# Performance work log

Measured on AMD Instinct MI355X. Metric: run time of the kernel, lower is better.

The kernel has to match this reference:

```python
import jax, jax.numpy as jnp
import numpy as np


def _relative_position_index(w):
    # Deterministic Swin relative-position index, shape [w*w, w*w], values in [0, (2w-1)^2)
    coords_h = np.arange(w)
    coords_w = np.arange(w)
    coords = np.stack(np.meshgrid(coords_h, coords_w, indexing="ij"))  # [2, w, w]
    coords = coords.reshape(2, -1)                                      # [2, w*w]
    rel = coords[:, :, None] - coords[:, None, :]                       # [2, N, N]
    rel = rel.transpose(1, 2, 0).copy()                                 # [N, N, 2]
    rel[:, :, 0] += w - 1
    rel[:, :, 1] += w - 1
    rel[:, :, 0] *= 2 * w - 1
    return jnp.asarray(rel.sum(-1), dtype=jnp.int32)


def setup_inputs() -> dict:
    key = jax.random.key(0)
    ks = jax.random.split(key, 7)
    BS, N, C, H, W = 4096, 49, 384, 12, 7
    NW = 64  # number of windows per image
    x = jax.random.normal(ks[0], (BS, N, C), dtype=jnp.float32)
    # Swin shift mask: 0 where attention allowed, -100 where blocked
    u = jax.random.uniform(ks[1], (NW, N, N))
    mask = jnp.where(u < 0.5, 0.0, -100.0).astype(jnp.float32)
    qkv_w = jax.random.normal(ks[2], (C, 3 * C), dtype=jnp.float32) * (C ** -0.5)
    qkv_b = jax.random.normal(ks[3], (3 * C,), dtype=jnp.float32) * 0.02
    proj_w = jax.random.normal(ks[4], (C, C), dtype=jnp.float32) * (C ** -0.5)
    proj_b = jax.random.normal(ks[5], (C,), dtype=jnp.float32) * 0.02
    bias_table = jax.random.normal(ks[6], ((2 * W - 1) ** 2, H), dtype=jnp.float32) * 0.02
    return {"x": x, "mask": mask, "qkv_w": qkv_w, "qkv_b": qkv_b,
            "proj_w": proj_w, "proj_b": proj_b, "bias_table": bias_table,
            "n_heads": 12, "window_size": 7}


def reference(x, mask, qkv_w, qkv_b, proj_w, proj_b, bias_table, n_heads, window_size):
    BS, N, C = x.shape
    Hh = n_heads
    hd = C // Hh
    scale = hd ** -0.5
    rpi = _relative_position_index(window_size)  # [N, N] int

    qkv = x @ qkv_w + qkv_b                       # [BS, N, 3C]
    qkv = qkv.reshape(BS, N, 3, Hh, hd).transpose(2, 0, 3, 1, 4)  # [3, BS, H, N, hd]
    q, k, v = qkv[0], qkv[1], qkv[2]

    attn = jnp.einsum("bhnd,bhmd->bhnm", q, k) * scale   # [BS, H, N, N]
    # relative position bias gather: [N*N, H] -> [H, N, N]
    rpb = bias_table[rpi.reshape(-1)].reshape(N, N, Hh).transpose(2, 0, 1)
    attn = attn + rpb[None]

    nw = mask.shape[0]
    attn = attn.reshape(BS // nw, nw, Hh, N, N) + mask[None, :, None]
    attn = attn.reshape(BS, Hh, N, N)

    attn = jax.nn.softmax(attn, axis=-1)
    out = jnp.einsum("bhnm,bhmd->bhnd", attn, v)          # [BS, H, N, hd]
    out = out.transpose(0, 2, 1, 3).reshape(BS, N, C)
    return out @ proj_w + proj_b
```

## Files before the change

### kernel.cpp

```cpp
#include <hip/hip_runtime.h>
#include <hip/hip_bf16.h>


typedef __attribute__((ext_vector_type(8))) short bf16x8;
typedef __attribute__((ext_vector_type(4))) float f32x4;

#define SEQ_N  49
#define CH     384
#define QKV_N  1152
#define HDIM   32
#define UNIT_ROWS 3136

__device__ __forceinline__ unsigned short f2b(float f) {
    union { float f; unsigned int u; } v; v.f = f;
    return (unsigned short)((v.u + 0x7FFFu + ((v.u >> 16) & 1u)) >> 16);
}

__device__ __forceinline__ bf16x8 ld8(const unsigned short* p) {
    return *(const bf16x8*)p;
}

__device__ __forceinline__ void gload16(const unsigned short* g, unsigned short* l) {
    __builtin_amdgcn_global_load_lds(
        (const __attribute__((address_space(1))) unsigned int*)g,
        (__attribute__((address_space(3))) unsigned int*)l, 16, 0, 0);
}

__device__ __forceinline__ int xcd_swizzle(int orig, int T) {
    int q = T >> 3, r = T & 7;
    int xcd = orig & 7, idx = orig >> 3;
    return (xcd < r ? xcd * (q + 1) : r * (q + 1) + (xcd - r) * q) + idx;
}

__global__ __launch_bounds__(256) void k_cvt_w(const float* __restrict__ wq,
        const float* __restrict__ wp, unsigned short* __restrict__ oq,
        unsigned short* __restrict__ op)
{
    int t = blockIdx.x * 256 + threadIdx.x;
    if (t < QKV_N * CH) {
        int n = t / CH, k = t - n * CH;
        oq[t] = f2b(wq[(size_t)k * QKV_N + n]);
    }
    if (t < CH * CH) {
        int n = t / CH, k = t - n * CH;
        op[t] = f2b(wp[(size_t)k * CH + n]);
    }
}

__global__ __launch_bounds__(256) void k_cvt(const float* __restrict__ in,
        unsigned short* __restrict__ outp, int n8)
{
    int stride = gridDim.x * 256;
    for (int i = blockIdx.x * 256 + threadIdx.x; i < n8; i += stride) {
        const float4* p = (const float4*)(in + (size_t)i * 8);
        float4 a = p[0], b = p[1];
        uint4 v;
        v.x = (unsigned)f2b(a.x) | ((unsigned)f2b(a.y) << 16);
        v.y = (unsigned)f2b(a.z) | ((unsigned)f2b(a.w) << 16);
        v.z = (unsigned)f2b(b.x) | ((unsigned)f2b(b.y) << 16);
        v.w = (unsigned)f2b(b.z) | ((unsigned)f2b(b.w) << 16);
        *(uint4*)(outp + (size_t)i * 8) = v;
    }
}

template<int OUTF32>
__global__ __launch_bounds__(256) void k_gemm(
        const unsigned short* __restrict__ A, int lda,
        const unsigned short* __restrict__ Bt, int K,
        const float* __restrict__ bias,
        unsigned short* __restrict__ Cb, float* __restrict__ Cf, int ldc,
        int M, int ntiles, int mtiles)
{
    __shared__ unsigned short As[128 * 32];
    __shared__ unsigned short Bs[128 * 32];
    const int wg = xcd_swizzle(blockIdx.x, mtiles * ntiles);
    const int m0 = (wg / ntiles) * 128;
    const int n0 = (wg % ntiles) * 128;
    const int tid = threadIdx.x;
    const int lane = tid & 63, wid = tid >> 6;
    const int wm = (wid >> 1) * 64, wn = (wid & 1) * 64;
    const int l15 = lane & 15, g = lane >> 4;

    f32x4 acc[4][4];
#pragma unroll
    for (int a = 0; a < 4; ++a)
#pragma unroll
        for (int b = 0; b < 4; ++b) acc[a][b] = (f32x4){0.f, 0.f, 0.f, 0.f};

    const int r0 = wid * 16 + (lane >> 2);
    const int kofs = (lane & 3) * 8;
    int ra0 = m0 + r0;       if (ra0 > M - 1) ra0 = M - 1;
    int ra1 = m0 + 64 + r0;  if (ra1 > M - 1) ra1 = M - 1;
    const unsigned short* a0p = A + (size_t)ra0 * lda + kofs;
    const unsigned short* a1p = A + (size_t)ra1 * lda + kofs;
    const unsigned short* b0p = Bt + (size_t)(n0 + r0) * K + kofs;
    const unsigned short* b1p = Bt + (size_t)(n0 + 64 + r0) * K + kofs;
    unsigned short* la0 = As + wid * 512;
    unsigned short* la1 = As + 2048 + wid * 512;
    unsigned short* lb0 = Bs + wid * 512;
    unsigned short* lb1 = Bs + 2048 + wid * 512;

    for (int kt = 0; kt < K; kt += 32) {
        gload16(a0p, la0);
        gload16(a1p, la1);
        gload16(b0p, lb0);
        gload16(b1p, lb1);
        a0p += 32; a1p += 32; b0p += 32; b1p += 32;
        __syncthreads();
        bf16x8 af[4], bfr[4];
#pragma unroll
        for (int mt = 0; mt < 4; ++mt)
            af[mt] = ld8(&As[(wm + mt * 16 + l15) * 32 + g * 8]);
#pragma unroll
        for (int nt = 0; nt < 4; ++nt)
            bfr[nt] = ld8(&Bs[(wn + nt * 16 + l15) * 32 + g * 8]);
#pragma unroll
        for (int mt = 0; mt < 4; ++mt)
#pragma unroll
            for (int nt = 0; nt < 4; ++nt)
                acc[mt][nt] = __builtin_amdgcn_mfma_f32_16x16x32_bf16(
                        af[mt], bfr[nt], acc[mt][nt], 0, 0, 0);
        __syncthreads();
    }

#pragma unroll
    for (int mt = 0; mt < 4; ++mt)
#pragma unroll
        for (int nt = 0; nt < 4; ++nt) {
            int col = n0 + wn + nt * 16 + l15;
            float bb = bias[col];
#pragma unroll
            for (int r = 0; r < 4; ++r) {
                int row = m0 + wm + mt * 16 + g * 4 + r;
                if (row < M) {
                    if (OUTF32)
                        Cf[(size_t)row * ldc + col] = acc[mt][nt][r] + bb;
                    else
                        Cb[(size_t)row * ldc + col] = f2b(acc[mt][nt][r] + bb);
                }
            }
        }
}

__global__ __launch_bounds__(256) void k_attn(unsigned short* __restrict__ qkv,
        const float* __restrict__ mask, const float* __restrict__ btab, int win_base)
{
    extern __shared__ unsigned short sm[];
    const int tid = threadIdx.x;
    const int lane = tid & 63, wv = tid >> 6;
    const int l15 = lane & 15, g = lane >> 4;
    const int pair = blockIdx.x * 4 + wv;
    const int winloc = pair / 12;
    const int h = pair - winloc * 12;
    const int wimg = (win_base + winloc) & 63;
    const int co = h * HDIM;
    unsigned short* Vt = sm + wv * 6912;
    unsigned short* Pw = Vt + 32 * 72;
    unsigned short* src = qkv + (size_t)winloc * SEQ_N * QKV_N;

    for (int t = lane; t < 32 * 16; t += 64) {
        int c = t >> 4, kk = 48 + (t & 15);
        Vt[c * 72 + kk] = 0;
    }
    for (int t = lane; t < 49 * 4; t += 64) {
        int row = t >> 2, cb = (t & 3) * 8;
        const unsigned short* vp = src + (size_t)row * QKV_N + 768 + co + cb;
        ushort4 a = ((const ushort4*)vp)[0];
        ushort4 b = ((const ushort4*)vp)[1];
        Vt[(cb + 0) * 72 + row] = a.x; Vt[(cb + 1) * 72 + row] = a.y;
        Vt[(cb + 2) * 72 + row] = a.z; Vt[(cb + 3) * 72 + row] = a.w;
        Vt[(cb + 4) * 72 + row] = b.x; Vt[(cb + 5) * 72 + row] = b.y;
        Vt[(cb + 6) * 72 + row] = b.z; Vt[(cb + 7) * 72 + row] = b.w;
    }

    bf16x8 qf[4], kf[4];
#pragma unroll
    for (int mt = 0; mt < 4; ++mt) {
        int r = mt * 16 + l15; if (r > 48) r = 48;
        qf[mt] = ld8(src + (size_t)r * QKV_N + co + g * 8);
    }
#pragma unroll
    for (int nt = 0; nt < 4; ++nt) {
        int r = nt * 16 + l15; if (r > 48) r = 48;
        kf[nt] = ld8(src + (size_t)r * QKV_N + CH + co + g * 8);
    }

    f32x4 sa[4][4];
#pragma unroll
    for (int mt = 0; mt < 4; ++mt)
#pragma unroll
        for (int nt = 0; nt < 4; ++nt) sa[mt][nt] = (f32x4){0.f, 0.f, 0.f, 0.f};
#pragma unroll
    for (int mt = 0; mt < 4; ++mt)
#pragma unroll
        for (int nt = 0; nt < 4; ++nt)
            sa[mt][nt] = __builtin_amdgcn_mfma_f32_16x16x32_bf16(
                    qf[mt], kf[nt], sa[mt][nt], 0, 0, 0);

    int jj[4], jh[4], jw4[4];
#pragma unroll
    for (int nt = 0; nt < 4; ++nt) {
        int j = nt * 16 + l15;
        jj[nt] = j; jh[nt] = j / 7; jw4[nt] = j - (j / 7) * 7;
    }
    const float scale = 0.17677669529663687f;
#pragma unroll
    for (int mt = 0; mt < 4; ++mt) {
#pragma unroll
        for (int r = 0; r < 4; ++r) {
            int i = mt * 16 + g * 4 + r;
            int ic = i < 49 ? i : 48;
            int ih = ic / 7, iw = ic - (ic / 7) * 7;
            const float* mrow = mask + (size_t)wimg * 2401 + ic * 49;
            float sv[4];
#pragma unroll
            for (int nt = 0; nt < 4; ++nt) {
                float s = sa[mt][nt][r];
                if (jj[nt] < 49) {
                    int idx = (ih - jh[nt] + 6) * 13 + (iw - jw4[nt] + 6);
                    s = s * scale + btab[idx * 12 + h] + mrow[jj[nt]];
                } else s = -1e30f;
                sv[nt] = s;
            }
            float mx = fmaxf(fmaxf(sv[0], sv[1]), fmaxf(sv[2], sv[3]));
#pragma unroll
            for (int d = 1; d < 16; d <<= 1) mx = fmaxf(mx, __shfl_xor(mx, d));
            float sum = 0.f;
#pragma unroll
            for (int nt = 0; nt < 4; ++nt) { sv[nt] = __expf(sv[nt] - mx); sum += sv[nt]; }
#pragma unroll
            for (int d = 1; d < 16; d <<= 1) sum += __shfl_xor(sum, d);
            float inv = 1.0f / sum;
#pragma unroll
            for (int nt = 0; nt < 4; ++nt)
                Pw[i * 72 + nt * 16 + l15] = f2b(sv[nt] * inv);
        }
    }
    __syncthreads();

    f32x4 oa[4][2];
#pragma unroll
    for (int mt = 0; mt < 4; ++mt)
#pragma unroll
        for (int nt = 0; nt < 2; ++nt) oa[mt][nt] = (f32x4){0.f, 0.f, 0.f, 0.f};
#pragma unroll
    for (int ks = 0; ks < 2; ++ks) {
        bf16x8 pf[4];
#pragma unroll
        for (int mt = 0; mt < 4; ++mt)
            pf[mt] = ld8(Pw + (mt * 16 + l15) * 72 + ks * 32 + g * 8);
#pragma unroll
        for (int nt = 0; nt < 2; ++nt) {
            bf16x8 vf = ld8(Vt + (nt * 16 + l15) * 72 + ks * 32 + g * 8);
#pragma unroll
            for (int mt = 0; mt < 4; ++mt)
                oa[mt][nt] = __builtin_amdgcn_mfma_f32_16x16x32_bf16(
                        pf[mt], vf, oa[mt][nt], 0, 0, 0);
        }
    }

#pragma unroll
    for (int mt = 0; mt < 4; ++mt)
#pragma unroll
        for (int r = 0; r < 4; ++r) {
            int i = mt * 16 + g * 4 + r;
            if (i < 49) {
#pragma unroll
                for (int nt = 0; nt < 2; ++nt)
                    src[(size_t)i * QKV_N + co + nt * 16 + l15] = f2b(oa[mt][nt][r]);
            }
        }
}

extern "C" void kernel_launch(void* const* d_in, const int* in_sizes, int n_in,
                              void* d_out, int out_size, void* d_ws, size_t ws_size,
                              hipStream_t stream) {
    const float* x      = (const float*)d_in[0];
    const float* mask   = (const float*)d_in[1];
    const float* qkv_w  = (const float*)d_in[2];
    const float* qkv_b  = (const float*)d_in[3];
    const float* proj_w = (const float*)d_in[4];
    const float* proj_b = (const float*)d_in[5];
    const float* btab   = (const float*)d_in[6];
    float* out = (float*)d_out;

    unsigned short* wq_bt = (unsigned short*)d_ws;
    unsigned short* wp_bt = wq_bt + QKV_N * CH;
    unsigned short* base  = wp_bt + CH * CH;
    const size_t fixed = (size_t)(QKV_N * CH + CH * CH) * 2;
    const size_t unit  = (size_t)UNIT_ROWS * (CH + QKV_N) * 2;
    if (ws_size < fixed + unit) return;
    int upc = (int)((ws_size - fixed) / unit);
    if (upc > 64) upc = 64;
    unsigned short* xb  = base;
    unsigned short* qkv = base + (size_t)upc * UNIT_ROWS * CH;

    const int smem2 = 4 * 6912 * 2;
    hipFuncSetAttribute(reinterpret_cast<const void*>(k_attn),
                        hipFuncAttributeMaxDynamicSharedMemorySize, smem2);

    dim3 blk(256);
    k_cvt_w<<<dim3((QKV_N * CH + 255) / 256), blk, 0, stream>>>(qkv_w, proj_w, wq_bt, wp_bt);

    for (int u0 = 0; u0 < 64; u0 += upc) {
        int units = (64 - u0) < upc ? (64 - u0) : upc;
        int m_base = u0 * UNIT_ROWS;
        int Mc = units * UNIT_ROWS;
        int mtiles = (Mc + 127) / 128;
        k_cvt<<<dim3(2048), blk, 0, stream>>>(x + (size_t)m_base * CH, xb, Mc * 48);
        k_gemm<0><<<dim3(mtiles * 9), blk, 0, stream>>>(
                xb, CH, wq_bt, CH, qkv_b, qkv, nullptr, QKV_N, Mc, 9, mtiles);
        k_attn<<<dim3(units * 192), blk, smem2, stream>>>(qkv, mask, btab, u0);
        k_gemm<1><<<dim3(mtiles * 3), blk, 0, stream>>>(
                qkv, QKV_N, wp_bt, CH, proj_b, nullptr, out + (size_t)m_base * CH,
                CH, Mc, 3, mtiles);
    }
}
```

Before: 1.050 ms.

## Double-buffer LDS tiles in GEMM to overlap global loads with MFMA

The GEMM kernel now keeps two LDS buffers for its A and B tiles. It issues the global-to-LDS loads for the next K-slice before running the MFMAs on the current one, and needs only one barrier per iteration instead of two. The goal is to hide global load latency behind compute. In exchange, LDS use doubles, which may lower occupancy.

```diff
diff --git a/kernel.cpp b/kernel.cpp
--- a/kernel.cpp
+++ b/kernel.cpp
@@ -71,8 +71,8 @@
         unsigned short* __restrict__ Cb, float* __restrict__ Cf, int ldc,
         int M, int ntiles, int mtiles)
 {
-    __shared__ unsigned short As[128 * 32];
-    __shared__ unsigned short Bs[128 * 32];
+    __shared__ unsigned short As[2][128 * 32];
+    __shared__ unsigned short Bs[2][128 * 32];
     const int wg = xcd_swizzle(blockIdx.x, mtiles * ntiles);
     const int m0 = (wg / ntiles) * 128;
     const int n0 = (wg % ntiles) * 128;
@@ -95,25 +95,27 @@
     const unsigned short* a1p = A + (size_t)ra1 * lda + kofs;
     const unsigned short* b0p = Bt + (size_t)(n0 + r0) * K + kofs;
     const unsigned short* b1p = Bt + (size_t)(n0 + 64 + r0) * K + kofs;
-    unsigned short* la0 = As + wid * 512;
-    unsigned short* la1 = As + 2048 + wid * 512;
-    unsigned short* lb0 = Bs + wid * 512;
-    unsigned short* lb1 = Bs + 2048 + wid * 512;
-
-    for (int kt = 0; kt < K; kt += 32) {
-        gload16(a0p, la0);
-        gload16(a1p, la1);
-        gload16(b0p, lb0);
-        gload16(b1p, lb1);
-        a0p += 32; a1p += 32; b0p += 32; b1p += 32;
-        __syncthreads();
+    const int lo = wid * 512;
+
+    gload16(a0p, &As[0][lo]);
+    gload16(a1p, &As[0][2048 + lo]);
+    gload16(b0p, &Bs[0][lo]);
+    gload16(b1p, &Bs[0][2048 + lo]);
+    __syncthreads();
+
+    int cur = 0;
+    for (int kt = 32; kt < K; kt += 32) {
+        gload16(a0p + kt, &As[cur ^ 1][lo]);
+        gload16(a1p + kt, &As[cur ^ 1][2048 + lo]);
+        gload16(b0p + kt, &Bs[cur ^ 1][lo]);
+        gload16(b1p + kt, &Bs[cur ^ 1][2048 + lo]);
         bf16x8 af[4], bfr[4];
 #pragma unroll
         for (int mt = 0; mt < 4; ++mt)
-            af[mt] = ld8(&As[(wm + mt * 16 + l15) * 32 + g * 8]);
+            af[mt] = ld8(&As[cur][(wm + mt * 16 + l15) * 32 + g * 8]);
 #pragma unroll
         for (int nt = 0; nt < 4; ++nt)
-            bfr[nt] = ld8(&Bs[(wn + nt * 16 + l15) * 32 + g * 8]);
+            bfr[nt] = ld8(&Bs[cur][(wn + nt * 16 + l15) * 32 + g * 8]);
 #pragma unroll
         for (int mt = 0; mt < 4; ++mt)
 #pragma unroll
@@ -121,6 +123,22 @@
                 acc[mt][nt] = __builtin_amdgcn_mfma_f32_16x16x32_bf16(
                         af[mt], bfr[nt], acc[mt][nt], 0, 0, 0);
         __syncthreads();
+        cur ^= 1;
+    }
+    {
+        bf16x8 af[4], bfr[4];
+#pragma unroll
+        for (int mt = 0; mt < 4; ++mt)
+            af[mt] = ld8(&As[cur][(wm + mt * 16 + l15) * 32 + g * 8]);
+#pragma unroll
+        for (int nt = 0; nt < 4; ++nt)
+            bfr[nt] = ld8(&Bs[cur][(wn + nt * 16 + l15) * 32 + g * 8]);
+#pragma unroll
+        for (int mt = 0; mt < 4; ++mt)
+#pragma unroll
+            for (int nt = 0; nt < 4; ++nt)
+                acc[mt][nt] = __builtin_amdgcn_mfma_f32_16x16x32_bf16(
+                        af[mt], bfr[nt], acc[mt][nt], 0, 0, 0);
     }
 
 #pragma unroll
```

Result: no change. 1.045 ms (-0.5%).

## Load GEMM MFMA fragments directly from global memory, dropping LDS staging

Applied to the files above, without the earlier changes.

The GEMM kernel no longer stages A and B tiles through shared memory with global_load_lds and barriers. Each lane now reads its MFMA fragments straight from global memory, relying on L1/L2 for reuse, and the K loop is unrolled by two. This removes both __syncthreads per K step and the LDS traffic. In exchange, each wave issues its own global loads, so data is fetched redundantly across waves and the loads are less coalesced (16-byte segments spread across rows).

```diff
diff --git a/kernel.cpp b/kernel.cpp
--- a/kernel.cpp
+++ b/kernel.cpp
@@ -18,12 +18,6 @@
 
 __device__ __forceinline__ bf16x8 ld8(const unsigned short* p) {
     return *(const bf16x8*)p;
-}
-
-__device__ __forceinline__ void gload16(const unsigned short* g, unsigned short* l) {
-    __builtin_amdgcn_global_load_lds(
-        (const __attribute__((address_space(1))) unsigned int*)g,
-        (__attribute__((address_space(3))) unsigned int*)l, 16, 0, 0);
 }
 
 __device__ __forceinline__ int xcd_swizzle(int orig, int T) {
@@ -71,8 +65,6 @@
         unsigned short* __restrict__ Cb, float* __restrict__ Cf, int ldc,
         int M, int ntiles, int mtiles)
 {
-    __shared__ unsigned short As[128 * 32];
-    __shared__ unsigned short Bs[128 * 32];
     const int wg = xcd_swizzle(blockIdx.x, mtiles * ntiles);
     const int m0 = (wg / ntiles) * 128;
     const int n0 = (wg % ntiles) * 128;
@@ -81,46 +73,37 @@
     const int wm = (wid >> 1) * 64, wn = (wid & 1) * 64;
     const int l15 = lane & 15, g = lane >> 4;
 
+    const unsigned short* ap[4];
+    const unsigned short* bp[4];
+#pragma unroll
+    for (int mt = 0; mt < 4; ++mt) {
+        int r = m0 + wm + mt * 16 + l15;
+        if (r > M - 1) r = M - 1;
+        ap[mt] = A + (size_t)r * lda + g * 8;
+    }
+#pragma unroll
+    for (int nt = 0; nt < 4; ++nt)
+        bp[nt] = Bt + (size_t)(n0 + wn + nt * 16 + l15) * K + g * 8;
+
     f32x4 acc[4][4];
 #pragma unroll
     for (int a = 0; a < 4; ++a)
 #pragma unroll
         for (int b = 0; b < 4; ++b) acc[a][b] = (f32x4){0.f, 0.f, 0.f, 0.f};
 
-    const int r0 = wid * 16 + (lane >> 2);
-    const int kofs = (lane & 3) * 8;
-    int ra0 = m0 + r0;       if (ra0 > M - 1) ra0 = M - 1;
-    int ra1 = m0 + 64 + r0;  if (ra1 > M - 1) ra1 = M - 1;
-    const unsigned short* a0p = A + (size_t)ra0 * lda + kofs;
-    const unsigned short* a1p = A + (size_t)ra1 * lda + kofs;
-    const unsigned short* b0p = Bt + (size_t)(n0 + r0) * K + kofs;
-    const unsigned short* b1p = Bt + (size_t)(n0 + 64 + r0) * K + kofs;
-    unsigned short* la0 = As + wid * 512;
-    unsigned short* la1 = As + 2048 + wid * 512;
-    unsigned short* lb0 = Bs + wid * 512;
-    unsigned short* lb1 = Bs + 2048 + wid * 512;
-
+#pragma unroll 2
     for (int kt = 0; kt < K; kt += 32) {
-        gload16(a0p, la0);
-        gload16(a1p, la1);
-        gload16(b0p, lb0);
-        gload16(b1p, lb1);
-        a0p += 32; a1p += 32; b0p += 32; b1p += 32;
-        __syncthreads();
         bf16x8 af[4], bfr[4];
 #pragma unroll
-        for (int mt = 0; mt < 4; ++mt)
-            af[mt] = ld8(&As[(wm + mt * 16 + l15) * 32 + g * 8]);
-#pragma unroll
-        for (int nt = 0; nt < 4; ++nt)
-            bfr[nt] = ld8(&Bs[(wn + nt * 16 + l15) * 32 + g * 8]);
+        for (int mt = 0; mt < 4; ++mt) af[mt] = ld8(ap[mt] + kt);
+#pragma unroll
+        for (int nt = 0; nt < 4; ++nt) bfr[nt] = ld8(bp[nt] + kt);
 #pragma unroll
         for (int mt = 0; mt < 4; ++mt)
 #pragma unroll
             for (int nt = 0; nt < 4; ++nt)
                 acc[mt][nt] = __builtin_amdgcn_mfma_f32_16x16x32_bf16(
                         af[mt], bfr[nt], acc[mt][nt], 0, 0, 0);
-        __syncthreads();
     }
 
 #pragma unroll
```

Measured after the change: 1.460 ms. 1.39x slower.

## Triple-buffer LDS tiles in GEMM to overlap global loads with MFMA

Applied to the files above, without the earlier changes.

Replaces the single-buffered load/sync/compute loop in the bf16 GEMM with a three-stage ring of LDS buffers. Global-to-LDS loads are issued two k-steps ahead, and explicit vmcnt waits plus raw s_barriers stand in for the old full __syncthreads pairs. This is meant to hide global memory latency behind the MFMA work. In exchange, LDS use per block triples to 48KB, which may reduce occupancy, and correctness now depends on the hand-written waitcnt counts.

```diff
diff --git a/kernel.cpp b/kernel.cpp
--- a/kernel.cpp
+++ b/kernel.cpp
@@ -71,8 +71,8 @@
         unsigned short* __restrict__ Cb, float* __restrict__ Cf, int ldc,
         int M, int ntiles, int mtiles)
 {
-    __shared__ unsigned short As[128 * 32];
-    __shared__ unsigned short Bs[128 * 32];
+    __shared__ unsigned short As[3 * 4096];
+    __shared__ unsigned short Bs[3 * 4096];
     const int wg = xcd_swizzle(blockIdx.x, mtiles * ntiles);
     const int m0 = (wg / ntiles) * 128;
     const int n0 = (wg % ntiles) * 128;
@@ -95,33 +95,64 @@
     const unsigned short* a1p = A + (size_t)ra1 * lda + kofs;
     const unsigned short* b0p = Bt + (size_t)(n0 + r0) * K + kofs;
     const unsigned short* b1p = Bt + (size_t)(n0 + 64 + r0) * K + kofs;
-    unsigned short* la0 = As + wid * 512;
-    unsigned short* la1 = As + 2048 + wid * 512;
-    unsigned short* lb0 = Bs + wid * 512;
-    unsigned short* lb1 = Bs + 2048 + wid * 512;
-
-    for (int kt = 0; kt < K; kt += 32) {
-        gload16(a0p, la0);
-        gload16(a1p, la1);
-        gload16(b0p, lb0);
-        gload16(b1p, lb1);
-        a0p += 32; a1p += 32; b0p += 32; b1p += 32;
-        __syncthreads();
-        bf16x8 af[4], bfr[4];
-#pragma unroll
-        for (int mt = 0; mt < 4; ++mt)
-            af[mt] = ld8(&As[(wm + mt * 16 + l15) * 32 + g * 8]);
-#pragma unroll
-        for (int nt = 0; nt < 4; ++nt)
-            bfr[nt] = ld8(&Bs[(wn + nt * 16 + l15) * 32 + g * 8]);
-#pragma unroll
-        for (int mt = 0; mt < 4; ++mt)
-#pragma unroll
-            for (int nt = 0; nt < 4; ++nt)
-                acc[mt][nt] = __builtin_amdgcn_mfma_f32_16x16x32_bf16(
-                        af[mt], bfr[nt], acc[mt][nt], 0, 0, 0);
-        __syncthreads();
-    }
+    const int lo = wid * 512;
+
+#define STAGE(kt, buf) do {                                   \
+        gload16(a0p + (kt), &As[(buf) * 4096 + lo]);          \
+        gload16(a1p + (kt), &As[(buf) * 4096 + 2048 + lo]);   \
+        gload16(b0p + (kt), &Bs[(buf) * 4096 + lo]);          \
+        gload16(b1p + (kt), &Bs[(buf) * 4096 + 2048 + lo]);   \
+    } while (0)
+
+#define COMPUTE(buf) do {                                                     \
+        bf16x8 af[4], bfr[4];                                                 \
+        _Pragma("unroll")                                                     \
+        for (int mt = 0; mt < 4; ++mt)                                        \
+            af[mt] = ld8(&As[(buf) * 4096 + (wm + mt * 16 + l15) * 32 + g * 8]); \
+        _Pragma("unroll")                                                     \
+        for (int nt = 0; nt < 4; ++nt)                                        \
+            bfr[nt] = ld8(&Bs[(buf) * 4096 + (wn + nt * 16 + l15) * 32 + g * 8]); \
+        _Pragma("unroll")                                                     \
+        for (int mt = 0; mt < 4; ++mt)                                        \
+            _Pragma("unroll")                                                 \
+            for (int nt = 0; nt < 4; ++nt)                                    \
+                acc[mt][nt] = __builtin_amdgcn_mfma_f32_16x16x32_bf16(        \
+                        af[mt], bfr[nt], acc[mt][nt], 0, 0, 0);               \
+    } while (0)
+
+    const int nsteps = K >> 5;
+
+    STAGE(0, 0);
+    STAGE(32, 1);
+
+    int cur = 0;
+    for (int t = 0; t < nsteps - 2; ++t) {
+        int pf = cur + 2; if (pf >= 3) pf -= 3;
+        STAGE((t + 2) * 32, pf);
+        __builtin_amdgcn_sched_barrier(0);
+        asm volatile("s_waitcnt vmcnt(8)" ::: "memory");
+        __builtin_amdgcn_sched_barrier(0);
+        __builtin_amdgcn_s_barrier();
+        __builtin_amdgcn_sched_barrier(0);
+        COMPUTE(cur);
+        __builtin_amdgcn_sched_barrier(0);
+        __builtin_amdgcn_s_barrier();
+        __builtin_amdgcn_sched_barrier(0);
+        cur = (cur == 2) ? 0 : cur + 1;
+    }
+    asm volatile("s_waitcnt vmcnt(4)" ::: "memory");
+    __builtin_amdgcn_sched_barrier(0);
+    __builtin_amdgcn_s_barrier();
+    __builtin_amdgcn_sched_barrier(0);
+    COMPUTE(cur);
+    cur = (cur == 2) ? 0 : cur + 1;
+    asm volatile("s_waitcnt vmcnt(0)" ::: "memory");
+    __builtin_amdgcn_sched_barrier(0);
+    __builtin_amdgcn_s_barrier();
+    __builtin_amdgcn_sched_barrier(0);
+    COMPUTE(cur);
+#undef STAGE
+#undef COMPUTE
 
 #pragma unroll
     for (int mt = 0; mt < 4; ++mt)
```

Measured after the change: 1.039 ms. About the same (-1.0%).
